# Kernel tuning notes

Hardware: AMD Instinct MI355X
Metric: run time of the kernel (lower is better)

Reference implementation:

```python
import jax, jax.numpy as jnp
import numpy as np

B, S, H = 4, 2048, 1024
NH, HD = 16, 64
FF = 4 * H
EPS = 1e-5


def _layernorm(x, g, b):
    m = jnp.mean(x, axis=-1, keepdims=True)
    v = jnp.mean((x - m) ** 2, axis=-1, keepdims=True)
    return (x - m) * jax.lax.rsqrt(v + EPS) * g + b


def setup_inputs() -> dict:
    key = jax.random.key(0)
    ks = jax.random.split(key, 12)
    std = 1.0 / np.sqrt(H)
    inp = {
        "x": jax.random.normal(ks[0], (B, S, H), dtype=jnp.float32),
        "attention_mask": jnp.ones((B, S), dtype=bool),
        "Wq": jax.random.normal(ks[1], (H, H), dtype=jnp.float32) * std,
        "bq": jnp.zeros((H,), dtype=jnp.float32),
        "Wk": jax.random.normal(ks[2], (H, H), dtype=jnp.float32) * std,
        "bk": jnp.zeros((H,), dtype=jnp.float32),
        "Wv": jax.random.normal(ks[3], (H, H), dtype=jnp.float32) * std,
        "bv": jnp.zeros((H,), dtype=jnp.float32),
        "Wo": jax.random.normal(ks[4], (H, H), dtype=jnp.float32) * std,
        "bo": jnp.zeros((H,), dtype=jnp.float32),
        "g1": jnp.ones((H,), dtype=jnp.float32),
        "b1": jnp.zeros((H,), dtype=jnp.float32),
        "g2": jnp.ones((H,), dtype=jnp.float32),
        "b2": jnp.zeros((H,), dtype=jnp.float32),
        "Wm1": jax.random.normal(ks[5], (FF, H), dtype=jnp.float32) * std,
        "bm1": jnp.zeros((FF,), dtype=jnp.float32),
        "Wm2": jax.random.normal(ks[6], (H, FF), dtype=jnp.float32) * (1.0 / np.sqrt(FF)),
        "bm2": jnp.zeros((H,), dtype=jnp.float32),
    }
    return inp


def reference(x, attention_mask, Wq, bq, Wk, bk, Wv, bv, Wo, bo,
              g1, b1, g2, b2, Wm1, bm1, Wm2, bm2):
    scale = 1.0 / np.sqrt(HD)
    normed = _layernorm(x, g1, b1)
    # torch Linear: y = x @ W.T + b
    q = (normed @ Wq.T + bq).reshape(B, S, NH, HD)
    k = (normed @ Wk.T + bk).reshape(B, S, NH, HD)
    v = (normed @ Wv.T + bv).reshape(B, S, NH, HD)
    # scores: [B, NH, S, S]
    scores = jnp.einsum("bqhd,bkhd->bhqk", q, k) * scale
    scores = jnp.where(attention_mask[:, None, None, :], scores, -jnp.inf)
    attn = jax.nn.softmax(scores, axis=-1)
    out = jnp.einsum("bhqk,bkhd->bqhd", attn, v).reshape(B, S, H)
    out = out @ Wo.T + bo
    x = x + out
    h = _layernorm(x, g2, b2)
    h = jax.nn.gelu(h @ Wm1.T + bm1, approximate=False) @ Wm2.T + bm2
    return x + h
```

## Files before the change

### kernel.cpp

```cpp
#include <hip/hip_runtime.h>
#include <math.h>


typedef unsigned short u16;
typedef unsigned int   u32;
typedef __attribute__((ext_vector_type(4)))  float f32x4;
typedef __attribute__((ext_vector_type(16))) float f32x16;
typedef __attribute__((ext_vector_type(8)))  short short8;

__device__ __forceinline__ u16 f2bf(float f){
  union { float f; u32 u; } v; v.f = f;
  u32 u = v.u;
  return (u16)((u + 0x7fffu + ((u >> 16) & 1u)) >> 16);
}
__device__ __forceinline__ float bf2f(u16 h){
  union { u32 u; float f; } v; v.u = ((u32)h) << 16;
  return v.f;
}

__device__ __forceinline__ void async16(const u16* g, u16* l){
  __builtin_amdgcn_global_load_lds((const __attribute__((address_space(1))) u32*)g,
                                   (__attribute__((address_space(3))) u32*)l, 16, 0, 0);
}

__device__ __forceinline__ u32 cvt_pk_bf16(float lo, float hi){
  u32 r;
  asm("v_cvt_pk_bf16_f32 %0, %1, %2" : "=v"(r) : "v"(lo), "v"(hi));
  return r;
}

__device__ __forceinline__ short8 frag4(u32 a, u32 b, u32 c, u32 d){
  union { u32 u[4]; short8 s; } x;
  x.u[0] = a; x.u[1] = b; x.u[2] = c; x.u[3] = d;
  return x.s;
}

__global__ __launch_bounds__(256) void k_cvt_all(
    const float* __restrict__ Wq, const float* __restrict__ Wk,
    const float* __restrict__ Wv, const float* __restrict__ Wo,
    const float* __restrict__ Wm1, const float* __restrict__ Wm2,
    const float* __restrict__ bq, const float* __restrict__ bk,
    const float* __restrict__ bv,
    u16* __restrict__ wqkv, u16* __restrict__ wo,
    u16* __restrict__ wm1, u16* __restrict__ wm2, float* __restrict__ bqkv){
  int c = blockIdx.x * 256 + threadIdx.x;
  const float* src; u16* dst;
  if      (c <  262144){ src = Wq  + c*4;             dst = wqkv + c*4; }
  else if (c <  524288){ src = Wk  + (c-262144)*4;    dst = wqkv + 1048576 + (c-262144)*4; }
  else if (c <  786432){ src = Wv  + (c-524288)*4;    dst = wqkv + 2097152 + (c-524288)*4; }
  else if (c < 1048576){ src = Wo  + (c-786432)*4;    dst = wo  + (c-786432)*4; }
  else if (c < 2097152){ src = Wm1 + (c-1048576)*4;   dst = wm1 + (c-1048576)*4; }
  else if (c < 3145728){ src = Wm2 + (c-2097152)*4;   dst = wm2 + (c-2097152)*4; }
  else if (c < 3146496){
    int i = (c - 3145728)*4;
    const float* bsrc = i < 1024 ? bq + i : (i < 2048 ? bk + i - 1024 : bv + i - 2048);
    *(float4*)(bqkv + i) = *(const float4*)bsrc;
    return;
  } else return;
  float4 v = *(const float4*)src;
  ushort4 o; o.x = f2bf(v.x); o.y = f2bf(v.y); o.z = f2bf(v.z); o.w = f2bf(v.w);
  *(ushort4*)dst = o;
}

__global__ __launch_bounds__(256) void k_ln(const float* __restrict__ x,
                                            const float* __restrict__ g,
                                            const float* __restrict__ b,
                                            u16* __restrict__ out){
  int row = blockIdx.x;
  int t = threadIdx.x;
  const float* xr = x + (size_t)row * 1024;
  float4 v = ((const float4*)xr)[t];
  float s = v.x + v.y + v.z + v.w;
  float q = v.x*v.x + v.y*v.y + v.z*v.z + v.w*v.w;
  #pragma unroll
  for (int off = 1; off < 64; off <<= 1){
    s += __shfl_xor(s, off);
    q += __shfl_xor(q, off);
  }
  __shared__ float ps[4], pq[4];
  int w = t >> 6, l = t & 63;
  if (l == 0){ ps[w] = s; pq[w] = q; }
  __syncthreads();
  s = ps[0] + ps[1] + ps[2] + ps[3];
  q = pq[0] + pq[1] + pq[2] + pq[3];
  float mean = s * (1.0f/1024.0f);
  float var  = q * (1.0f/1024.0f) - mean*mean;
  float rstd = rsqrtf(var + 1e-5f);
  float4 gv = ((const float4*)g)[t];
  float4 bv = ((const float4*)b)[t];
  ushort4 o;
  o.x = f2bf((v.x - mean)*rstd*gv.x + bv.x);
  o.y = f2bf((v.y - mean)*rstd*gv.y + bv.y);
  o.z = f2bf((v.z - mean)*rstd*gv.z + bv.z);
  o.w = f2bf((v.w - mean)*rstd*gv.w + bv.w);
  ((ushort4*)(out + (size_t)row * 1024))[t] = o;
}

__global__ __launch_bounds__(256) void k_vt(const u16* __restrict__ QKV,
                                            u16* __restrict__ VT){
  __shared__ u16 lt[64][66];
  const int t = threadIdx.x;
  const int bh = blockIdx.x >> 5, sblk = blockIdx.x & 31;
  const size_t rowbase = (size_t)(bh >> 4) * 2048;
  const int hd = (bh & 15) * 64;
  const u16* src = QKV + (rowbase + sblk*64) * 3072 + hd + 2048;
  u16* dst = VT + (size_t)bh * 131072 + sblk*64;
  #pragma unroll
  for (int i = 0; i < 2; i++){
    int r = i*32 + (t >> 3), c0 = (t & 7) * 8;
    short8 v = *(const short8*)(src + (size_t)r * 3072 + c0);
    #pragma unroll
    for (int j = 0; j < 8; j++) lt[r][c0 + j] = (u16)v[j];
  }
  __syncthreads();
  #pragma unroll
  for (int i = 0; i < 2; i++){
    int d = i*32 + (t >> 3), toff = (t & 7) * 8;
    short8 o;
    #pragma unroll
    for (int j = 0; j < 8; j++) o[j] = (short)lt[toff + j][d];
    *(short8*)(dst + (size_t)d * 2048 + toff) = o;
  }
}

#define MF(FRB, FCB) { \
  _Pragma("unroll") for (int ks = 0; ks < 2; ks++) \
  _Pragma("unroll") for (int fr = 0; fr < 4; fr++) \
  _Pragma("unroll") for (int fc = 0; fc < 2; fc++) \
    acc[(FRB)+fr][(FCB)+fc] = __builtin_amdgcn_mfma_f32_16x16x32_bf16( \
        a[fr][ks], b[fc][ks], acc[(FRB)+fr][(FCB)+fc], 0, 0, 0); }

#define STAGE(BUF, H, KT) { \
  async16(hbase[H] + (size_t)gr_[0]*K + (KT)*64 + gc_[0], &lds[BUF][H][t*8]); \
  async16(hbase[H] + (size_t)gr_[1]*K + (KT)*64 + gc_[1], &lds[BUF][H][4096 + t*8]); }

#define BARRIER() { __builtin_amdgcn_s_barrier(); __builtin_amdgcn_sched_barrier(0); }

template<int EPI>
__global__ __launch_bounds__(512, 2) void k_gemm256(const u16* __restrict__ A,
    const u16* __restrict__ Bw, const float* __restrict__ bias, void* __restrict__ Cp,
    const float* __restrict__ res, int M, int N, int K, int ntn){
  __shared__ __align__(16) u16 lds[2][4][8192];
  const int t = threadIdx.x;
  const int l = t & 63, w = t >> 6;
  const int wm = w >> 2, wn = w & 3;
  const int lr = l & 15, g = l >> 4;

  const int nwg = gridDim.x;
  int wg = blockIdx.x;
  if (!(nwg & 7)) wg = (wg & 7) * (nwg >> 3) + (wg >> 3);
  const int bm = (wg / ntn) * 256, bn = (wg % ntn) * 256;

  int gr_[2], gc_[2];
  #pragma unroll
  for (int i = 0; i < 2; i++){
    int ch = i*512 + t;
    int sr = ch >> 7, sc = (ch >> 6) & 1, r = (ch >> 2) & 15;
    int c  = ((ch & 3) * 8) ^ (((r >> 3) & 1) << 4);
    gr_[i] = sr*16 + r;
    gc_[i] = sc*32 + c;
  }
  const u16* hbase[4] = { A  + (size_t) bm        * K,
                          A  + (size_t)(bm + 128) * K,
                          Bw + (size_t) bn        * K,
                          Bw + (size_t)(bn + 128) * K };

  const int roff = lr*32 + ((g*8) ^ (((lr >> 3) & 1) << 4));

  f32x4 acc[8][4];
  #pragma unroll
  for (int i = 0; i < 8; i++)
    #pragma unroll
    for (int j = 0; j < 4; j++)
      acc[i][j] = (f32x4)(0.0f);
  short8 a[4][2], b[2][2];

  #define LDA(HB) { _Pragma("unroll") for (int fr = 0; fr < 4; fr++) \
    _Pragma("unroll") for (int ks = 0; ks < 2; ks++) \
      a[fr][ks] = *(const short8*)((HB) + (fr*4 + wm*2 + ks)*512 + roff); }
  #define LDB(HB) { _Pragma("unroll") for (int fc = 0; fc < 2; fc++) \
    _Pragma("unroll") for (int ks = 0; ks < 2; ks++) \
      b[fc][ks] = *(const short8*)((HB) + ((fc*4 + wn)*2 + ks)*512 + roff); }

  const int NT = K >> 6;
  STAGE(0, 0, 0); STAGE(0, 2, 0); STAGE(0, 3, 0); STAGE(0, 1, 0);
  asm volatile("s_waitcnt vmcnt(4)" ::: "memory");
  BARRIER();

  for (int kt = 0; kt < NT; kt++){
    const int cu = kt & 1, nx = cu ^ 1;
    const u16* LA0 = lds[cu][0]; const u16* LA1 = lds[cu][1];
    const u16* LB0 = lds[cu][2]; const u16* LB1 = lds[cu][3];
    const bool pf = (kt + 1 < NT);
    LDA(LA0); LDB(LB0);
    if (pf) STAGE(nx, 0, kt+1);
    __builtin_amdgcn_s_setprio(1);
    MF(0, 0);
    __builtin_amdgcn_s_setprio(0);
    if (pf) asm volatile("s_waitcnt vmcnt(4)" ::: "memory");
    else    asm volatile("s_waitcnt vmcnt(2)" ::: "memory");
    BARRIER();
    LDB(LB1);
    if (pf) STAGE(nx, 2, kt+1);
    __builtin_amdgcn_s_setprio(1);
    MF(0, 2);
    __builtin_amdgcn_s_setprio(0);
    if (pf) asm volatile("s_waitcnt vmcnt(4)" ::: "memory");
    else    asm volatile("s_waitcnt vmcnt(0)" ::: "memory");
    BARRIER();
    LDA(LA1);
    if (pf) STAGE(nx, 3, kt+1);
    __builtin_amdgcn_s_setprio(1);
    MF(4, 2);
    __builtin_amdgcn_s_setprio(0);
    BARRIER();
    LDB(LB0);
    if (pf) STAGE(nx, 1, kt+1);
    __builtin_amdgcn_s_setprio(1);
    MF(4, 0);
    __builtin_amdgcn_s_setprio(0);
    if (pf) asm volatile("s_waitcnt vmcnt(4)" ::: "memory");
    BARRIER();
  }

  const int m0 = bm + wm*16 + g*4;
  const int n0 = bn + wn*16 + lr;
  #pragma unroll
  for (int fc = 0; fc < 4; fc++){
    int col = n0 + fc*64;
    float bb = bias[col];
    #pragma unroll
    for (int fr = 0; fr < 8; fr++){
      int rowb = m0 + fr*32;
      #pragma unroll
      for (int r = 0; r < 4; r++){
        float v = acc[fr][fc][r] + bb;
        if constexpr (EPI == 2)
          v = 0.5f * v * (1.0f + erff(v * 0.70710678118654752f));
        size_t idx = (size_t)(rowb + r) * N + col;
        if constexpr (EPI == 1)
          ((float*)Cp)[idx] = v + res[idx];
        else
          ((u16*)Cp)[idx] = f2bf(v);
      }
    }
  }
}
#undef MF
#undef STAGE
#undef LDA
#undef LDB
#undef BARRIER

__global__ __launch_bounds__(256) void k_flash(const u16* __restrict__ QKV,
                                               const u16* __restrict__ VT,
                                               u16* __restrict__ O){
  constexpr int QSTR = 3072, OSTR = 1024;
  __shared__ __align__(16) u16 lK [2][64*64];
  __shared__ __align__(16) u16 lVT[2][64*64];

  const int t = threadIdx.x;
  const int l = t & 63, w = t >> 6;
  const int c31 = l & 31, h = l >> 5;
  const int bx = blockIdx.x;
  const int qt = bx & 15, bh = bx >> 4;
  const size_t rowbase = (size_t)(bh >> 4) * 2048;
  const int hd = (bh & 15) * 64;
  const u16* Qg  = QKV + rowbase * QSTR + hd;
  const u16* Kg  = Qg + 1024;
  const u16* VTg = VT + (size_t)bh * 131072;
  u16* Og = O + rowbase * OSTR + hd;
  const int qrow0 = qt * 128 + w * 32;

  short8 qf[4];
  #pragma unroll
  for (int d0 = 0; d0 < 4; d0++){
    short8 v = *(const short8*)(Qg + (size_t)(qrow0 + c31) * QSTR + d0*16 + 8*h);
    #pragma unroll
    for (int j = 0; j < 8; j++)
      v[j] = (short)f2bf(bf2f((u16)v[j]) * 0.18033688011112042f);
    qf[d0] = v;
  }

  f32x16 oa0 = (f32x16)(0.0f), oa1 = (f32x16)(0.0f);
  float m_run = -1e30f, l_run = 0.0f;
  const int rb = (c31 & 7) << 4;

  #pragma unroll
  for (int i = 0; i < 2; i++){
    int idx = i*256 + t;
    int row = idx >> 3, c = (idx & 7) ^ (row & 7);
    async16(Kg  + (size_t)row * QSTR + c*8, &lK [0][idx*8]);
    async16(VTg + (size_t)row * 2048 + c*8, &lVT[0][idx*8]);
  }
  __syncthreads();

  for (int kt = 0; kt < 32; kt++){
    const int cur = kt & 1;
    const char* lKc = (const char*)&lK[cur][0];
    const char* lVc = (const char*)&lVT[cur][0];

    if (kt < 31){
      #pragma unroll
      for (int i = 0; i < 2; i++){
        int idx = i*256 + t;
        int row = idx >> 3, c = (idx & 7) ^ (row & 7);
        async16(Kg  + (size_t)((kt+1)*64 + row) * QSTR + c*8, &lK [cur^1][idx*8]);
        async16(VTg + (size_t)row * 2048 + (kt+1)*64 + c*8,   &lVT[cur^1][idx*8]);
      }
    }

    f32x16 sa0 = (f32x16)(0.0f), sa1 = (f32x16)(0.0f);
    #pragma unroll
    for (int d0 = 0; d0 < 4; d0++){
      int cb = (d0*32 + 16*h) ^ rb;
      short8 kf0 = *(const short8*)(lKc + c31*128 + cb);
      short8 kf1 = *(const short8*)(lKc + (32+c31)*128 + cb);
      sa0 = __builtin_amdgcn_mfma_f32_32x32x16_bf16(kf0, qf[d0], sa0, 0, 0, 0);
      sa1 = __builtin_amdgcn_mfma_f32_32x32x16_bf16(kf1, qf[d0], sa1, 0, 0, 0);
    }

    float pm = fmaxf(sa0[0], sa0[1]);
    #pragma unroll
    for (int r = 2; r < 16; r++) pm = fmaxf(pm, sa0[r]);
    #pragma unroll
    for (int r = 0; r < 16; r++) pm = fmaxf(pm, sa1[r]);
    pm = fmaxf(pm, __shfl_xor(pm, 32));
    if (!__all(pm <= m_run + 8.0f)){
      float mnew = fmaxf(m_run, pm);
      float alpha = exp2f(m_run - mnew);
      m_run = mnew;
      l_run *= alpha;
      #pragma unroll
      for (int r = 0; r < 16; r++){
        int qr = (r&3) + 8*(r>>2) + 4*h;
        float ar = __shfl(alpha, qr);
        oa0[r] *= ar; oa1[r] *= ar;
      }
    }
    float rs = 0.0f;
    #pragma unroll
    for (int r = 0; r < 16; r++){ float p = exp2f(sa0[r] - m_run); sa0[r] = p; rs += p; }
    #pragma unroll
    for (int r = 0; r < 16; r++){ float p = exp2f(sa1[r] - m_run); sa1[r] = p; rs += p; }
    rs += __shfl_xor(rs, 32);
    l_run += rs;

    short8 pa[4];
    {
      u32 a0 = cvt_pk_bf16(sa0[0], sa0[1]),  a1 = cvt_pk_bf16(sa0[2], sa0[3]);
      u32 a2 = cvt_pk_bf16(sa0[4], sa0[5]),  a3 = cvt_pk_bf16(sa0[6], sa0[7]);
      asm("v_permlane32_swap_b32 %0, %1" : "+v"(a0), "+v"(a2));
      asm("v_permlane32_swap_b32 %0, %1" : "+v"(a1), "+v"(a3));
      pa[0] = frag4(a0, a1, a2, a3);
      u32 b0 = cvt_pk_bf16(sa0[8], sa0[9]),  b1 = cvt_pk_bf16(sa0[10], sa0[11]);
      u32 b2 = cvt_pk_bf16(sa0[12], sa0[13]), b3 = cvt_pk_bf16(sa0[14], sa0[15]);
      asm("v_permlane32_swap_b32 %0, %1" : "+v"(b0), "+v"(b2));
      asm("v_permlane32_swap_b32 %0, %1" : "+v"(b1), "+v"(b3));
      pa[1] = frag4(b0, b1, b2, b3);
      u32 c0 = cvt_pk_bf16(sa1[0], sa1[1]),  c1 = cvt_pk_bf16(sa1[2], sa1[3]);
      u32 c2 = cvt_pk_bf16(sa1[4], sa1[5]),  c3 = cvt_pk_bf16(sa1[6], sa1[7]);
      asm("v_permlane32_swap_b32 %0, %1" : "+v"(c0), "+v"(c2));
      asm("v_permlane32_swap_b32 %0, %1" : "+v"(c1), "+v"(c3));
      pa[2] = frag4(c0, c1, c2, c3);
      u32 d0 = cvt_pk_bf16(sa1[8], sa1[9]),  d1 = cvt_pk_bf16(sa1[10], sa1[11]);
      u32 d2 = cvt_pk_bf16(sa1[12], sa1[13]), d3 = cvt_pk_bf16(sa1[14], sa1[15]);
      asm("v_permlane32_swap_b32 %0, %1" : "+v"(d0), "+v"(d2));
      asm("v_permlane32_swap_b32 %0, %1" : "+v"(d1), "+v"(d3));
      pa[3] = frag4(d0, d1, d2, d3);
    }

    #pragma unroll
    for (int ks = 0; ks < 4; ks++){
      int cb = (ks*32 + 16*h) ^ rb;
      short8 vb0 = *(const short8*)(lVc + c31*128 + cb);
      short8 vb1 = *(const short8*)(lVc + (32+c31)*128 + cb);
      oa0 = __builtin_amdgcn_mfma_f32_32x32x16_bf16(pa[ks], vb0, oa0, 0, 0, 0);
      oa1 = __builtin_amdgcn_mfma_f32_32x32x16_bf16(pa[ks], vb1, oa1, 0, 0, 0);
    }
    __syncthreads();
  }

  float linv = 1.0f / l_run;
  #pragma unroll
  for (int r = 0; r < 16; r++){
    int qr = (r&3) + 8*(r>>2) + 4*h;
    float lr2 = __shfl(linv, qr);
    size_t ro = (size_t)(qrow0 + qr) * OSTR;
    Og[ro + c31]      = f2bf(oa0[r] * lr2);
    Og[ro + 32 + c31] = f2bf(oa1[r] * lr2);
  }
}

extern "C" void kernel_launch(void* const* d_in, const int* in_sizes, int n_in,
                              void* d_out, int out_size, void* d_ws, size_t ws_size,
                              hipStream_t stream){
  const float* x   = (const float*)d_in[0];
  const float* Wq  = (const float*)d_in[2];
  const float* bq  = (const float*)d_in[3];
  const float* Wk  = (const float*)d_in[4];
  const float* bk  = (const float*)d_in[5];
  const float* Wv  = (const float*)d_in[6];
  const float* bv  = (const float*)d_in[7];
  const float* Wo  = (const float*)d_in[8];
  const float* bo  = (const float*)d_in[9];
  const float* g1  = (const float*)d_in[10];
  const float* b1  = (const float*)d_in[11];
  const float* g2  = (const float*)d_in[12];
  const float* b2  = (const float*)d_in[13];
  const float* Wm1 = (const float*)d_in[14];
  const float* bm1 = (const float*)d_in[15];
  const float* Wm2 = (const float*)d_in[16];
  const float* bm2 = (const float*)d_in[17];

  const size_t MB = 1024 * 1024;
  char* ws = (char*)d_ws;
  u16*   wqkv = (u16*)(ws + 0*MB);
  u16*   wo   = (u16*)(ws + 6*MB);
  u16*   wm1  = (u16*)(ws + 8*MB);
  u16*   wm2  = (u16*)(ws + 16*MB);
  float* bqkv = (float*)(ws + 24*MB);
  u16*   nrm  = (u16*)(ws + 25*MB);
  u16*   vt   = (u16*)(ws + 25*MB);
  u16*   qkvb = (u16*)(ws + 41*MB);
  u16*   attn = (u16*)(ws + 89*MB);
  float* x2   = (float*)(ws + 105*MB);
  u16*   h1   = (u16*)(ws + 41*MB);
  u16*   nrm2 = (u16*)(ws + 73*MB);


  k_cvt_all<<<12291, 256, 0, stream>>>(Wq, Wk, Wv, Wo, Wm1, Wm2, bq, bk, bv,
                                       wqkv, wo, wm1, wm2, bqkv);

  const int M = 8192;
  k_ln<<<M, 256, 0, stream>>>(x, g1, b1, nrm);
  k_gemm256<0><<<dim3(32*12), 512, 0, stream>>>(nrm, wqkv, bqkv, qkvb, nullptr, M, 3072, 1024, 12);
  k_vt<<<2048, 256, 0, stream>>>(qkvb, vt);
  k_flash<<<1024, 256, 0, stream>>>(qkvb, vt, attn);
  k_gemm256<1><<<dim3(32*4), 512, 0, stream>>>(attn, wo, bo, x2, x, M, 1024, 1024, 4);
  k_ln<<<M, 256, 0, stream>>>(x2, g2, b2, nrm);
  k_gemm256<2><<<dim3(32*16), 512, 0, stream>>>(nrm, wm1, bm1, h1, nullptr, M, 4096, 1024, 16);
  k_gemm256<1><<<dim3(32*4), 512, 0, stream>>>(h1, wm2, bm2, d_out, x2, M, 1024, 4096, 4);
}
```

Baseline: 467.0 us.

## Fuse V transpose into flash attention and enlarge query tile to 256

Removes the separate V-transpose kernel: flash attention now loads V rows from the QKV buffer into registers and writes them transposed into swizzled LDS after the PV MFMAs, overlapping with compute. Blocks grow to 512 threads covering 256 query rows, which halves the number of blocks and the K/V reload traffic per head. The block index is remapped to spread query tiles across heads, and s_setprio is raised around the MFMA sections. The cost is extra register pressure and scalar LDS stores inside the main loop.

New measurement: 474.1 us. No clear change (+1.5%).

```diff
diff --git a/kernel.cpp b/kernel.cpp
--- a/kernel.cpp
+++ b/kernel.cpp
@@ -7,6 +7,7 @@
 typedef __attribute__((ext_vector_type(4)))  float f32x4;
 typedef __attribute__((ext_vector_type(16))) float f32x16;
 typedef __attribute__((ext_vector_type(8)))  short short8;
+typedef __attribute__((ext_vector_type(4)))  short short4v;
 
 __device__ __forceinline__ u16 f2bf(float f){
   union { float f; u32 u; } v; v.f = f;
@@ -96,33 +97,6 @@
   ((ushort4*)(out + (size_t)row * 1024))[t] = o;
 }
 
-__global__ __launch_bounds__(256) void k_vt(const u16* __restrict__ QKV,
-                                            u16* __restrict__ VT){
-  __shared__ u16 lt[64][66];
-  const int t = threadIdx.x;
-  const int bh = blockIdx.x >> 5, sblk = blockIdx.x & 31;
-  const size_t rowbase = (size_t)(bh >> 4) * 2048;
-  const int hd = (bh & 15) * 64;
-  const u16* src = QKV + (rowbase + sblk*64) * 3072 + hd + 2048;
-  u16* dst = VT + (size_t)bh * 131072 + sblk*64;
-  #pragma unroll
-  for (int i = 0; i < 2; i++){
-    int r = i*32 + (t >> 3), c0 = (t & 7) * 8;
-    short8 v = *(const short8*)(src + (size_t)r * 3072 + c0);
-    #pragma unroll
-    for (int j = 0; j < 8; j++) lt[r][c0 + j] = (u16)v[j];
-  }
-  __syncthreads();
-  #pragma unroll
-  for (int i = 0; i < 2; i++){
-    int d = i*32 + (t >> 3), toff = (t & 7) * 8;
-    short8 o;
-    #pragma unroll
-    for (int j = 0; j < 8; j++) o[j] = (short)lt[toff + j][d];
-    *(short8*)(dst + (size_t)d * 2048 + toff) = o;
-  }
-}
-
 #define MF(FRB, FCB) { \
   _Pragma("unroll") for (int ks = 0; ks < 2; ks++) \
   _Pragma("unroll") for (int fr = 0; fr < 4; fr++) \
@@ -252,8 +226,7 @@
 #undef LDB
 #undef BARRIER
 
-__global__ __launch_bounds__(256) void k_flash(const u16* __restrict__ QKV,
-                                               const u16* __restrict__ VT,
+__global__ __launch_bounds__(512) void k_flash(const u16* __restrict__ QKV,
                                                u16* __restrict__ O){
   constexpr int QSTR = 3072, OSTR = 1024;
   __shared__ __align__(16) u16 lK [2][64*64];
@@ -262,15 +235,15 @@
   const int t = threadIdx.x;
   const int l = t & 63, w = t >> 6;
   const int c31 = l & 31, h = l >> 5;
-  const int bx = blockIdx.x;
-  const int qt = bx & 15, bh = bx >> 4;
+  const int rbx = ((blockIdx.x & 7) << 6) + (blockIdx.x >> 3);
+  const int qt = rbx & 7, bh = rbx >> 3;
   const size_t rowbase = (size_t)(bh >> 4) * 2048;
   const int hd = (bh & 15) * 64;
-  const u16* Qg  = QKV + rowbase * QSTR + hd;
-  const u16* Kg  = Qg + 1024;
-  const u16* VTg = VT + (size_t)bh * 131072;
+  const u16* Qg = QKV + rowbase * QSTR + hd;
+  const u16* Kg = Qg + 1024;
+  const u16* Vg = Qg + 2048;
   u16* Og = O + rowbase * OSTR + hd;
-  const int qrow0 = qt * 128 + w * 32;
+  const int qrow0 = qt * 256 + w * 32;
 
   short8 qf[4];
   #pragma unroll
@@ -284,33 +257,41 @@
 
   f32x16 oa0 = (f32x16)(0.0f), oa1 = (f32x16)(0.0f);
   float m_run = -1e30f, l_run = 0.0f;
+
+  const int vkv0 = 2*(t & 31), vdh = t >> 5;
   const int rb = (c31 & 7) << 4;
 
-  #pragma unroll
-  for (int i = 0; i < 2; i++){
-    int idx = i*256 + t;
-    int row = idx >> 3, c = (idx & 7) ^ (row & 7);
-    async16(Kg  + (size_t)row * QSTR + c*8, &lK [0][idx*8]);
-    async16(VTg + (size_t)row * 2048 + c*8, &lVT[0][idx*8]);
+  {
+    int row = t >> 3, c = (t & 7) ^ (row & 7);
+    async16(Kg + (size_t)row * QSTR + c*8, &lK[0][t*8]);
+    const u16* vs = Vg + (size_t)vkv0 * QSTR + vdh*4;
+    short4v v0 = *(const short4v*)(vs);
+    short4v v1 = *(const short4v*)(vs + QSTR);
+    #pragma unroll
+    for (int j = 0; j < 4; j++){
+      int d = vdh*4 + j;
+      u32 word = (u32)(u16)v0[j] | ((u32)(u16)v1[j] << 16);
+      *(u32*)((char*)&lVT[0][0] + d*128 + ((vkv0*2) ^ ((d&7)<<4))) = word;
+    }
   }
   __syncthreads();
 
+  short4v v0s, v1s;
   for (int kt = 0; kt < 32; kt++){
     const int cur = kt & 1;
     const char* lKc = (const char*)&lK[cur][0];
     const char* lVc = (const char*)&lVT[cur][0];
 
     if (kt < 31){
-      #pragma unroll
-      for (int i = 0; i < 2; i++){
-        int idx = i*256 + t;
-        int row = idx >> 3, c = (idx & 7) ^ (row & 7);
-        async16(Kg  + (size_t)((kt+1)*64 + row) * QSTR + c*8, &lK [cur^1][idx*8]);
-        async16(VTg + (size_t)row * 2048 + (kt+1)*64 + c*8,   &lVT[cur^1][idx*8]);
-      }
+      int row = t >> 3, c = (t & 7) ^ (row & 7);
+      async16(Kg + (size_t)((kt+1)*64 + row) * QSTR + c*8, &lK[cur^1][t*8]);
+      const u16* vs = Vg + (size_t)((kt+1)*64 + vkv0) * QSTR + vdh*4;
+      v0s = *(const short4v*)(vs);
+      v1s = *(const short4v*)(vs + QSTR);
     }
 
     f32x16 sa0 = (f32x16)(0.0f), sa1 = (f32x16)(0.0f);
+    __builtin_amdgcn_s_setprio(1);
     #pragma unroll
     for (int d0 = 0; d0 < 4; d0++){
       int cb = (d0*32 + 16*h) ^ rb;
@@ -319,6 +300,7 @@
       sa0 = __builtin_amdgcn_mfma_f32_32x32x16_bf16(kf0, qf[d0], sa0, 0, 0, 0);
       sa1 = __builtin_amdgcn_mfma_f32_32x32x16_bf16(kf1, qf[d0], sa1, 0, 0, 0);
     }
+    __builtin_amdgcn_s_setprio(0);
 
     float pm = fmaxf(sa0[0], sa0[1]);
     #pragma unroll
@@ -370,6 +352,7 @@
       pa[3] = frag4(d0, d1, d2, d3);
     }
 
+    __builtin_amdgcn_s_setprio(1);
     #pragma unroll
     for (int ks = 0; ks < 4; ks++){
       int cb = (ks*32 + 16*h) ^ rb;
@@ -377,6 +360,16 @@
       short8 vb1 = *(const short8*)(lVc + (32+c31)*128 + cb);
       oa0 = __builtin_amdgcn_mfma_f32_32x32x16_bf16(pa[ks], vb0, oa0, 0, 0, 0);
       oa1 = __builtin_amdgcn_mfma_f32_32x32x16_bf16(pa[ks], vb1, oa1, 0, 0, 0);
+    }
+    __builtin_amdgcn_s_setprio(0);
+
+    if (kt < 31){
+      #pragma unroll
+      for (int j = 0; j < 4; j++){
+        int d = vdh*4 + j;
+        u32 word = (u32)(u16)v0s[j] | ((u32)(u16)v1s[j] << 16);
+        *(u32*)((char*)&lVT[cur^1][0] + d*128 + ((vkv0*2) ^ ((d&7)<<4))) = word;
+      }
     }
     __syncthreads();
   }
@@ -421,13 +414,10 @@
   u16*   wm2  = (u16*)(ws + 16*MB);
   float* bqkv = (float*)(ws + 24*MB);
   u16*   nrm  = (u16*)(ws + 25*MB);
-  u16*   vt   = (u16*)(ws + 25*MB);
   u16*   qkvb = (u16*)(ws + 41*MB);
   u16*   attn = (u16*)(ws + 89*MB);
   float* x2   = (float*)(ws + 105*MB);
   u16*   h1   = (u16*)(ws + 41*MB);
-  u16*   nrm2 = (u16*)(ws + 73*MB);
-
 
   k_cvt_all<<<12291, 256, 0, stream>>>(Wq, Wk, Wv, Wo, Wm1, Wm2, bq, bk, bv,
                                        wqkv, wo, wm1, wm2, bqkv);
@@ -435,8 +425,7 @@
   const int M = 8192;
   k_ln<<<M, 256, 0, stream>>>(x, g1, b1, nrm);
   k_gemm256<0><<<dim3(32*12), 512, 0, stream>>>(nrm, wqkv, bqkv, qkvb, nullptr, M, 3072, 1024, 12);
-  k_vt<<<2048, 256, 0, stream>>>(qkvb, vt);
-  k_flash<<<1024, 256, 0, stream>>>(qkvb, vt, attn);
+  k_flash<<<512, 512, 0, stream>>>(qkvb, attn);
   k_gemm256<1><<<dim3(32*4), 512, 0, stream>>>(attn, wo, bo, x2, x, M, 1024, 1024, 4);
   k_ln<<<M, 256, 0, stream>>>(x2, g2, b2, nrm);
   k_gemm256<2><<<dim3(32*16), 512, 0, stream>>>(nrm, wm1, bm1, h1, nullptr, M, 4096, 1024, 16);
```
